# Kernel optimization log

Hardware: AMD Instinct MI355X
Metric: run time of the kernel (lower is better)

## Reference

```python
import jax, jax.numpy as jnp
import numpy as np

N, H, W, C = 2, 96, 96, 256
HEADS, P = 8, 25
DH = C // HEADS
HID = int(C * 4.0)


def _ln(x, g, b):
    m = jnp.mean(x, axis=-1, keepdims=True)
    v = jnp.var(x, axis=-1, keepdims=True)
    return (x - m) / jnp.sqrt(v + 1e-5) * g + b


def _deform_sample(value, loc, h, w):
    # value: (n, heads, h*w, dh); loc: (n, Lq, heads, P, 2) normalized to [0,1] (x,y)
    # Bilinear sampling with align_corners=False and zero padding, as in
    # grid_sample used by MSDeformAttn.
    n = value.shape[0]
    gx = loc[..., 0] * w - 0.5
    gy = loc[..., 1] * h - 0.5
    x0 = jnp.floor(gx)
    y0 = jnp.floor(gy)
    fx = gx - x0
    fy = gy - y0
    out = jnp.zeros((n, HEADS, gx.shape[1] * P, DH), dtype=value.dtype)
    for dx, dy in ((0, 0), (1, 0), (0, 1), (1, 1)):
        xi = x0 + dx
        yi = y0 + dy
        wgt = (fx if dx else 1.0 - fx) * (fy if dy else 1.0 - fy)
        valid = ((xi >= 0) & (xi <= w - 1) & (yi >= 0) & (yi <= h - 1)).astype(value.dtype)
        xi_c = jnp.clip(xi, 0, w - 1).astype(jnp.int32)
        yi_c = jnp.clip(yi, 0, h - 1).astype(jnp.int32)
        idx = yi_c * w + xi_c                                   # (n, Lq, heads, P)
        idx = jnp.transpose(idx, (0, 2, 1, 3)).reshape(n, HEADS, -1)
        g = jnp.take_along_axis(value, idx[..., None], axis=2)  # (n, heads, Lq*P, dh)
        wv = jnp.transpose(wgt * valid, (0, 2, 1, 3)).reshape(n, HEADS, -1, 1)
        out = out + g * wv
    return out


def setup_inputs() -> dict:
    key = jax.random.key(0)
    ks = jax.random.split(key, 20)
    s = 0.02
    inp = {
        'x': jax.random.normal(ks[0], (N, H, W, C), jnp.float32),
        'ref_points': jax.random.uniform(ks[1], (N, H * W, 1, 2), jnp.float32),
        'spatial_shapes': jnp.array([[H, W]], dtype=jnp.int32),
        'level_start_index': jnp.zeros((1,), dtype=jnp.int32),
        'ln1_g': jnp.ones((C,), jnp.float32),
        'ln1_b': jnp.zeros((C,), jnp.float32),
        'w_off': jax.random.normal(ks[2], (C, HEADS * P * 2), jnp.float32) * s,
        'b_off': jax.random.normal(ks[3], (HEADS * P * 2,), jnp.float32) * s,
        'w_attn': jax.random.normal(ks[4], (C, HEADS * P), jnp.float32) * s,
        'b_attn': jax.random.normal(ks[5], (HEADS * P,), jnp.float32) * s,
        'w_val': jax.random.normal(ks[6], (C, C), jnp.float32) * s,
        'b_val': jnp.zeros((C,), jnp.float32),
        'w_out': jax.random.normal(ks[7], (C, C), jnp.float32) * s,
        'b_out': jnp.zeros((C,), jnp.float32),
        'ln2_g': jnp.ones((C,), jnp.float32),
        'ln2_b': jnp.zeros((C,), jnp.float32),
        'w_fc1': jax.random.normal(ks[8], (C, HID), jnp.float32) * s,
        'b_fc1': jnp.zeros((HID,), jnp.float32),
        'w_fc2': jax.random.normal(ks[9], (HID, C), jnp.float32) * s,
        'b_fc2': jnp.zeros((C,), jnp.float32),
    }
    return inp


def reference(x, ref_points, spatial_shapes, level_start_index,
              ln1_g, ln1_b, w_off, b_off, w_attn, b_attn,
              w_val, b_val, w_out, b_out, ln2_g, ln2_b,
              w_fc1, b_fc1, w_fc2, b_fc2):
    n, h, w, c = x.shape
    lq = h * w
    shortcut = x
    # pre-norm + flatten to query
    q = _ln(x, ln1_g, ln1_b).reshape(n, lq, c)
    # MSDeformAttn (n_levels = 1)
    value = (q @ w_val + b_val).reshape(n, lq, HEADS, DH).transpose(0, 2, 1, 3)
    off = (q @ w_off + b_off).reshape(n, lq, HEADS, P, 2)
    aw = jax.nn.softmax((q @ w_attn + b_attn).reshape(n, lq, HEADS, P), axis=-1)
    norm = jnp.array([w, h], dtype=x.dtype)          # offsets normalized by (W, H)
    ref = ref_points[:, :, 0, :]                     # (n, Lq, 2)
    loc = ref[:, :, None, None, :] + off / norm      # (n, Lq, heads, P, 2)
    sampled = _deform_sample(value, loc, h, w).reshape(n, HEADS, lq, P, DH)
    attn = jnp.einsum('nqhp,nhqpd->nqhd', aw, sampled).reshape(n, lq, c)
    attn = attn @ w_out + b_out
    x1 = shortcut + attn.reshape(n, h, w, c)
    # MLP block
    y = _ln(x1, ln2_g, ln2_b)
    y = jax.nn.gelu(y @ w_fc1 + b_fc1, approximate=False) @ w_fc2 + b_fc2
    return x1 + y
```

## Files before the change

kernel.cpp:

```cpp
#include <hip/hip_runtime.h>
#include <hip/hip_bf16.h>
#include <math.h>

typedef __hip_bfloat16 bf16;
typedef __attribute__((ext_vector_type(8))) short short8;
typedef __attribute__((ext_vector_type(4))) float f32x4;

#define NB 2
#define HH 96
#define WW 96
#define CC 256
#define NHEADS 8
#define PP 25
#define DHH 32
#define HIDN 1024
#define LQ (HH*WW)
#define TT (NB*LQ)
#define NVC 896
#define TB 4

__device__ __forceinline__ float b2f(bf16 v){ return __bfloat162float(v); }
__device__ __forceinline__ bf16  f2b(float v){ return __float2bfloat16(v); }
__device__ __forceinline__ float lo_bf(unsigned u){ return __uint_as_float(u << 16); }
__device__ __forceinline__ float hi_bf(unsigned u){ return __uint_as_float(u & 0xffff0000u); }

__device__ __forceinline__ void gl2lds16(const void* g, void* l) {
    __builtin_amdgcn_global_load_lds(
        (const __attribute__((address_space(1))) unsigned int*)g,
        (__attribute__((address_space(3))) unsigned int*)l, 16, 0, 0);
}

__global__ __launch_bounds__(256) void prep_all(const float* __restrict__ w_val,
                                                const float* __restrict__ w_off,
                                                const float* __restrict__ w_attn,
                                                const float* __restrict__ w_fc1,
                                                const float* __restrict__ w_fc2,
                                                const float* __restrict__ w_out,
                                                const float* __restrict__ b_val,
                                                const float* __restrict__ b_off,
                                                const float* __restrict__ b_attn,
                                                bf16* __restrict__ wvcT,
                                                bf16* __restrict__ wfc1T,
                                                bf16* __restrict__ wfc2T,
                                                bf16* __restrict__ woutT,
                                                float* __restrict__ bvc)
{
    const int idx = blockIdx.x*256 + threadIdx.x;
    if (idx < 229376) {
        int n = idx >> 8, k = idx & 255;
        float v = (n < 256) ? w_val[(size_t)k*256 + n]
                : (n < 656) ? w_off[(size_t)k*400 + (n-256)]
                : (n < 856) ? w_attn[(size_t)k*200 + (n-656)] : 0.f;
        wvcT[idx] = f2b(v);
    } else if (idx < 491520) {
        int j = idx - 229376; int n = j >> 8, k = j & 255;
        wfc1T[j] = f2b(w_fc1[(size_t)k*1024 + n]);
    } else if (idx < 753664) {
        int j = idx - 491520; int n = j >> 10, k = j & 1023;
        wfc2T[j] = f2b(w_fc2[(size_t)k*256 + n]);
    } else if (idx < 819200) {
        int j = idx - 753664; int n = j >> 8, k = j & 255;
        woutT[j] = f2b(w_out[(size_t)k*256 + n]);
    }
    if (idx < NVC)
        bvc[idx] = (idx < 256) ? b_val[idx]
                 : (idx < 656) ? b_off[idx-256]
                 : (idx < 856) ? b_attn[idx-656] : 0.f;
}

__global__ __launch_bounds__(256) void ln_kernel(const float* __restrict__ x,
                                                 const float* __restrict__ g,
                                                 const float* __restrict__ b,
                                                 bf16* __restrict__ out)
{
    const int t = blockIdx.x*4 + (threadIdx.x >> 6);
    const int l = threadIdx.x & 63;
    const float4 v = *(const float4*)(x + (size_t)t*CC + l*4);
    float s  = v.x + v.y + v.z + v.w;
    float s2 = v.x*v.x + v.y*v.y + v.z*v.z + v.w*v.w;
    #pragma unroll
    for (int m = 1; m < 64; m <<= 1) { s += __shfl_xor(s, m); s2 += __shfl_xor(s2, m); }
    const float mean = s * (1.f/CC);
    const float var  = s2 * (1.f/CC) - mean*mean;
    const float rs   = 1.f / sqrtf(var + 1e-5f);
    const float4 gg = *(const float4*)(g + l*4);
    const float4 bb = *(const float4*)(b + l*4);
    bf16 o[4];
    o[0] = f2b((v.x-mean)*rs*gg.x + bb.x);
    o[1] = f2b((v.y-mean)*rs*gg.y + bb.y);
    o[2] = f2b((v.z-mean)*rs*gg.z + bb.z);
    o[3] = f2b((v.w-mean)*rs*gg.w + bb.w);
    *(uint2*)(out + (size_t)t*CC + l*4) = *(uint2*)o;
}

template<int EPI, int K, int N, int TM>
__global__ __launch_bounds__(256) void mfma_gemm(const bf16* __restrict__ A,
                                                 const bf16* __restrict__ Bt,
                                                 const float* __restrict__ bias,
                                                 void* __restrict__ outv,
                                                 const float* __restrict__ resid,
                                                 bf16* __restrict__ val_d)
{
    constexpr int AR  = TM/8;
    constexpr int TR  = AR + 16;
    constexpr int RPW = TR/4;
    constexpr int NJ  = (TM==128) ? 4 : 2;
    __shared__ short As[TM*64];
    __shared__ short Bs[128*64];
    const int tid = threadIdx.x;
    const int w = tid >> 6, l = tid & 63;
    const int bm = blockIdx.x, bn = blockIdx.y;

    const bf16* sbase[RPW];
    short*      lbase[RPW];
    {
        const int lrow = l >> 3;
        const int q    = (l & 7) ^ lrow;
        #pragma unroll
        for (int j = 0; j < RPW; j++) {
            int r = w*RPW + j;
            bool isA = r < AR;
            int rr = isA ? r : r - AR;
            int row = rr*8 + lrow;
            size_t grow = (size_t)(isA ? (bm*TM + row) : (bn*128 + row));
            sbase[j] = (isA ? A : Bt) + grow*K + q*8;
            lbase[j] = (isA ? As : Bs) + rr*512;
        }
    }

    const int mbase = (TM==128) ? 64*(w >> 1) : 0;
    const int nbase = (TM==128) ? 64*(w & 1)  : 32*w;

    int aoff[2][4], boff[2][NJ];
    #pragma unroll
    for (int s = 0; s < 2; s++) {
        const int q = s*4 + (l >> 4);
        #pragma unroll
        for (int i = 0; i < 4; i++) {
            int m = mbase + i*16 + (l & 15);
            aoff[s][i] = (m*8 + (q ^ (m & 7))) * 8;
        }
        #pragma unroll
        for (int j = 0; j < NJ; j++) {
            int n = nbase + j*16 + (l & 15);
            boff[s][j] = (n*8 + (q ^ (n & 7))) * 8;
        }
    }

    f32x4 acc[4][NJ];
    #pragma unroll
    for (int i = 0; i < 4; i++)
        #pragma unroll
        for (int j = 0; j < NJ; j++)
            acc[i][j] = (f32x4){0.f, 0.f, 0.f, 0.f};

    for (int k0 = 0; k0 < K; k0 += 64) {
        #pragma unroll
        for (int j = 0; j < RPW; j++)
            gl2lds16(sbase[j] + k0, lbase[j]);
        __syncthreads();
        #pragma unroll
        for (int s = 0; s < 2; s++) {
            short8 af[4], bfr[NJ];
            #pragma unroll
            for (int i = 0; i < 4; i++)  af[i]  = *(const short8*)(As + aoff[s][i]);
            #pragma unroll
            for (int j = 0; j < NJ; j++) bfr[j] = *(const short8*)(Bs + boff[s][j]);
            #pragma unroll
            for (int i = 0; i < 4; i++)
                #pragma unroll
                for (int j = 0; j < NJ; j++)
                    acc[i][j] = __builtin_amdgcn_mfma_f32_16x16x32_bf16(af[i], bfr[j], acc[i][j], 0, 0, 0);
        }
        __syncthreads();
    }

    const int row0 = bm*TM + mbase + (l >> 4)*4;
    const int col0 = bn*128 + nbase + (l & 15);
    #pragma unroll
    for (int i = 0; i < 4; i++) {
        #pragma unroll
        for (int j = 0; j < NJ; j++) {
            const int col = col0 + j*16;
            const float bs = bias[col];
            #pragma unroll
            for (int r = 0; r < 4; r++) {
                const int row = row0 + i*16 + r;
                float v = acc[i][j][r] + bs;
                size_t o = (size_t)row * N + col;
                if (EPI == 0) {
                    ((bf16*)outv)[o] = f2b(v);
                } else if (EPI == 2) {
                    ((bf16*)outv)[o] = f2b(0.5f * v * (1.f + erff(v * 0.70710678118654752f)));
                } else if (EPI == 3) {
                    ((float*)outv)[o] = v + resid[o];
                } else {
                    if (col < 256) val_d[(size_t)row*CC + col] = f2b(v);
                    else           ((bf16*)outv)[o] = f2b(v);
                }
            }
        }
    }
}

struct __align__(16) Tap { _Float16 w[4]; unsigned short i[4]; };

__global__ __launch_bounds__(256) void sample_kernel(const bf16* __restrict__ vc,
                                                     const bf16* __restrict__ val_d,
                                                     const float* __restrict__ refp,
                                                     bf16* __restrict__ samp)
{
    __shared__ Tap taps[TB*200];
    const int b = blockIdx.x;
    const int xcd = b & 7, sub = b >> 3;
    const int tbase = (xcd >> 2)*LQ + ((xcd & 3)*576 + sub)*TB;
    const int tid = threadIdx.x;

    {
        const int pair = tid >> 3;
        const int j    = tid & 7;
        const int tl   = pair >> 3;
        const int h    = pair & 7;
        const int t    = tbase + tl;
        const bf16* row = vc + (size_t)t*NVC;

        float lg[4];
        #pragma unroll
        for (int k = 0; k < 4; k++) {
            int p = j + 8*k;
            lg[k] = (p < PP) ? b2f(row[656 + h*25 + p]) : -1e30f;
        }
        float m = fmaxf(fmaxf(lg[0], lg[1]), fmaxf(lg[2], lg[3]));
        m = fmaxf(m, __shfl_xor(m, 1));
        m = fmaxf(m, __shfl_xor(m, 2));
        m = fmaxf(m, __shfl_xor(m, 4));
        float ex[4], s = 0.f;
        #pragma unroll
        for (int k = 0; k < 4; k++) {
            ex[k] = (j + 8*k < PP) ? expf(lg[k] - m) : 0.f;
            s += ex[k];
        }
        s += __shfl_xor(s, 1);
        s += __shfl_xor(s, 2);
        s += __shfl_xor(s, 4);
        const float inv = 1.f / s;

        const float rx96 = refp[(size_t)t*2 + 0]*96.f - 0.5f;
        const float ry96 = refp[(size_t)t*2 + 1]*96.f - 0.5f;
        const unsigned* offp = (const unsigned*)(row + 256 + h*50);

        #pragma unroll
        for (int k = 0; k < 4; k++) {
            const int p = j + 8*k;
            if (p >= PP) break;
            const float a = ex[k] * inv;
            const unsigned uo = offp[p];
            const float gx = rx96 + lo_bf(uo);
            const float gy = ry96 + hi_bf(uo);
            const float x0f = floorf(gx), y0f = floorf(gy);
            const float fx = gx - x0f, fy = gy - y0f;
            const int ix = (int)x0f, iy = (int)y0f;
            Tap tp;
            #pragma unroll
            for (int d = 0; d < 4; d++) {
                const int dx = d & 1, dy = d >> 1;
                const int xi = ix + dx, yi = iy + dy;
                const bool valid = (xi >= 0) & (xi <= WW-1) & (yi >= 0) & (yi <= HH-1);
                const int xc = min(max(xi, 0), WW-1);
                const int yc = min(max(yi, 0), HH-1);
                tp.i[d] = (unsigned short)(yc*WW + xc);
                tp.w[d] = (_Float16)(valid ? a * (dx ? fx : 1.f-fx) * (dy ? fy : 1.f-fy) : 0.f);
            }
            taps[tl*200 + h*25 + p] = tp;
        }
    }
    __syncthreads();

    const int tok = tid >> 6, l = tid & 63;
    const int h   = l >> 3;
    const int g4  = l & 7;
    const int c0  = h*DHH + g4*4;
    const int t   = tbase + tok;
    const int n   = (t >= LQ) ? 1 : 0;
    const bf16* pv = val_d + (size_t)n*LQ*CC + c0;
    const int pib = tok*200 + h*25;

    float a0 = 0.f, a1 = 0.f, a2 = 0.f, a3 = 0.f;
    for (int p = 0; p < PP; p++) {
        const uint4 tv = *((const uint4*)taps + (pib + p));
        const _Float16* wp_ = (const _Float16*)&tv;
        const unsigned short* ip_ = (const unsigned short*)&tv + 4;
        #pragma unroll
        for (int d = 0; d < 4; d++) {
            const float wt = (float)wp_[d];
            const uint2 vv = *(const uint2*)(pv + (size_t)ip_[d]*CC);
            a0 += wt*lo_bf(vv.x); a1 += wt*hi_bf(vv.x);
            a2 += wt*lo_bf(vv.y); a3 += wt*hi_bf(vv.y);
        }
    }
    bf16 o[4] = { f2b(a0), f2b(a1), f2b(a2), f2b(a3) };
    *(uint2*)(samp + (size_t)t*CC + c0) = *(uint2*)o;
}

extern "C" void kernel_launch(void* const* d_in, const int* in_sizes, int n_in,
                              void* d_out, int out_size, void* d_ws, size_t ws_size,
                              hipStream_t stream)
{
    const float* x      = (const float*)d_in[0];
    const float* refp   = (const float*)d_in[1];
    const float* ln1_g  = (const float*)d_in[4];
    const float* ln1_b  = (const float*)d_in[5];
    const float* w_off  = (const float*)d_in[6];
    const float* b_off  = (const float*)d_in[7];
    const float* w_attn = (const float*)d_in[8];
    const float* b_attn = (const float*)d_in[9];
    const float* w_val  = (const float*)d_in[10];
    const float* b_val  = (const float*)d_in[11];
    const float* w_out  = (const float*)d_in[12];
    const float* b_out  = (const float*)d_in[13];
    const float* ln2_g  = (const float*)d_in[14];
    const float* ln2_b  = (const float*)d_in[15];
    const float* w_fc1  = (const float*)d_in[16];
    const float* b_fc1  = (const float*)d_in[17];
    const float* w_fc2  = (const float*)d_in[18];
    const float* b_fc2  = (const float*)d_in[19];

    char* wsb = (char*)d_ws;
    bf16*  q     = (bf16*)(wsb + 0);
    bf16*  vc    = (bf16*)(wsb + 9437184);
    bf16*  samp  = (bf16*)(wsb + 42467328);
    float* x1    = (float*)(wsb + 51904512);
    bf16*  wvcT  = (bf16*)(wsb + 70778880);
    bf16*  wfc1T = (bf16*)(wsb + 71237632);
    bf16*  wfc2T = (bf16*)(wsb + 71761920);
    bf16*  woutT = (bf16*)(wsb + 72286208);
    float* bvc   = (float*)(wsb + 72417280);
    bf16*  val_d = (bf16*)(wsb + 72420864);
    bf16*  hid   = (bf16*)(wsb + 0);
    bf16*  y0    = samp;

    if (ws_size < 81858048) return;

    const dim3 blk(256);
    prep_all<<<dim3(3200), blk, 0, stream>>>(w_val, w_off, w_attn, w_fc1, w_fc2, w_out,
                                             b_val, b_off, b_attn,
                                             wvcT, wfc1T, wfc2T, woutT, bvc);
    ln_kernel<<<dim3(TT/4), blk, 0, stream>>>(x, ln1_g, ln1_b, q);
    mfma_gemm<4,256,NVC,128><<<dim3(TT/128, NVC/128), blk, 0, stream>>>(q, wvcT, bvc, (void*)vc, nullptr, val_d);
    sample_kernel<<<dim3(TT/TB), blk, 0, stream>>>(vc, val_d, refp, samp);
    mfma_gemm<3,256,CC,64><<<dim3(TT/64, CC/128), blk, 0, stream>>>(samp, woutT, b_out, (void*)x1, x, nullptr);
    ln_kernel<<<dim3(TT/4), blk, 0, stream>>>(x1, ln2_g, ln2_b, y0);
    mfma_gemm<2,256,HIDN,128><<<dim3(TT/128, HIDN/128), blk, 0, stream>>>(y0, wfc1T, b_fc1, (void*)hid, nullptr, nullptr);
    mfma_gemm<3,HIDN,CC,64><<<dim3(TT/64, CC/128), blk, 0, stream>>>(hid, wfc2T, b_fc2, d_out, x1, nullptr);
}
```

Before: 250.7 us.

## Merge bilinear taps into a per-head local weight grid before gathering values

For each (token, head) the sampler now computes the bounding box of all 25 sampling points. If the box fits in a 6x6 window, it scatter-adds the bilinear weights into a shared-memory grid using LDS atomics. The gather loop then reads each distinct pixel once, skipping zero-weight cells, instead of 100 separate tap loads. Wider boxes fall back to the original tap list. This adds an extra barrier, grid zeroing and atomic contention in exchange for far fewer global value gathers when offsets are small.

```diff
diff --git a/kernel.cpp b/kernel.cpp
--- a/kernel.cpp
+++ b/kernel.cpp
@@ -18,6 +18,7 @@
 #define TT (NB*LQ)
 #define NVC 896
 #define TB 4
+#define GW 6
 
 __device__ __forceinline__ float b2f(bf16 v){ return __bfloat162float(v); }
 __device__ __forceinline__ bf16  f2b(float v){ return __float2bfloat16(v); }
@@ -210,11 +211,16 @@
                                                      const float* __restrict__ refp,
                                                      bf16* __restrict__ samp)
 {
-    __shared__ Tap taps[TB*200];
+    __shared__ Tap   taps[TB*200];
+    __shared__ float sgrid[TB*8*36];
+    __shared__ int   smeta[TB*8];
     const int b = blockIdx.x;
     const int xcd = b & 7, sub = b >> 3;
     const int tbase = (xcd >> 2)*LQ + ((xcd & 3)*576 + sub)*TB;
     const int tid = threadIdx.x;
+
+    #pragma unroll
+    for (int i = tid; i < TB*8*36; i += 256) sgrid[i] = 0.f;
 
     {
         const int pair = tid >> 3;
@@ -234,44 +240,94 @@
         m = fmaxf(m, __shfl_xor(m, 1));
         m = fmaxf(m, __shfl_xor(m, 2));
         m = fmaxf(m, __shfl_xor(m, 4));
-        float ex[4], s = 0.f;
+        float aa[4], s = 0.f;
         #pragma unroll
         for (int k = 0; k < 4; k++) {
-            ex[k] = (j + 8*k < PP) ? expf(lg[k] - m) : 0.f;
-            s += ex[k];
+            aa[k] = (j + 8*k < PP) ? expf(lg[k] - m) : 0.f;
+            s += aa[k];
         }
         s += __shfl_xor(s, 1);
         s += __shfl_xor(s, 2);
         s += __shfl_xor(s, 4);
         const float inv = 1.f / s;
+        #pragma unroll
+        for (int k = 0; k < 4; k++) aa[k] *= inv;
 
         const float rx96 = refp[(size_t)t*2 + 0]*96.f - 0.5f;
         const float ry96 = refp[(size_t)t*2 + 1]*96.f - 0.5f;
         const unsigned* offp = (const unsigned*)(row + 256 + h*50);
-
+        float gxs[4], gys[4];
+        int mnx = 95, mxx = 0, mny = 95, mxy = 0;
         #pragma unroll
         for (int k = 0; k < 4; k++) {
             const int p = j + 8*k;
             if (p >= PP) break;
-            const float a = ex[k] * inv;
             const unsigned uo = offp[p];
-            const float gx = rx96 + lo_bf(uo);
-            const float gy = ry96 + hi_bf(uo);
-            const float x0f = floorf(gx), y0f = floorf(gy);
-            const float fx = gx - x0f, fy = gy - y0f;
-            const int ix = (int)x0f, iy = (int)y0f;
-            Tap tp;
-            #pragma unroll
-            for (int d = 0; d < 4; d++) {
-                const int dx = d & 1, dy = d >> 1;
-                const int xi = ix + dx, yi = iy + dy;
-                const bool valid = (xi >= 0) & (xi <= WW-1) & (yi >= 0) & (yi <= HH-1);
-                const int xc = min(max(xi, 0), WW-1);
-                const int yc = min(max(yi, 0), HH-1);
-                tp.i[d] = (unsigned short)(yc*WW + xc);
-                tp.w[d] = (_Float16)(valid ? a * (dx ? fx : 1.f-fx) * (dy ? fy : 1.f-fy) : 0.f);
+            gxs[k] = rx96 + lo_bf(uo);
+            gys[k] = ry96 + hi_bf(uo);
+            const int ix = (int)floorf(gxs[k]);
+            const int iy = (int)floorf(gys[k]);
+            mnx = min(mnx, min(max(ix,   0), WW-1));
+            mxx = max(mxx, min(max(ix+1, 0), WW-1));
+            mny = min(mny, min(max(iy,   0), HH-1));
+            mxy = max(mxy, min(max(iy+1, 0), HH-1));
+        }
+        mnx = min(mnx, __shfl_xor(mnx, 1)); mxx = max(mxx, __shfl_xor(mxx, 1));
+        mnx = min(mnx, __shfl_xor(mnx, 2)); mxx = max(mxx, __shfl_xor(mxx, 2));
+        mnx = min(mnx, __shfl_xor(mnx, 4)); mxx = max(mxx, __shfl_xor(mxx, 4));
+        mny = min(mny, __shfl_xor(mny, 1)); mxy = max(mxy, __shfl_xor(mxy, 1));
+        mny = min(mny, __shfl_xor(mny, 2)); mxy = max(mxy, __shfl_xor(mxy, 2));
+        mny = min(mny, __shfl_xor(mny, 4)); mxy = max(mxy, __shfl_xor(mxy, 4));
+        const int bw = mxx - mnx + 1, bh = mxy - mny + 1;
+        const int ok = (bw <= GW && bh <= GW) ? 1 : 0;
+        if (j == 0)
+            smeta[pair] = mnx | (mny << 7) | (bw << 14) | (bh << 21) | (ok << 28);
+
+        __syncthreads();
+
+        if (ok) {
+            float* gp = sgrid + pair*36;
+            #pragma unroll
+            for (int k = 0; k < 4; k++) {
+                const int p = j + 8*k;
+                if (p >= PP) break;
+                const float a = aa[k];
+                const float x0f = floorf(gxs[k]), y0f = floorf(gys[k]);
+                const float fx = gxs[k] - x0f, fy = gys[k] - y0f;
+                const int ix = (int)x0f, iy = (int)y0f;
+                #pragma unroll
+                for (int d = 0; d < 4; d++) {
+                    const int dx = d & 1, dy = d >> 1;
+                    const int xi = ix + dx, yi = iy + dy;
+                    const bool valid = (xi >= 0) & (xi <= WW-1) & (yi >= 0) & (yi <= HH-1);
+                    const int xc = min(max(xi, 0), WW-1);
+                    const int yc = min(max(yi, 0), HH-1);
+                    const float wt = valid ? a * (dx ? fx : 1.f-fx) * (dy ? fy : 1.f-fy) : 0.f;
+                    atomicAdd(&gp[(yc - mny)*GW + (xc - mnx)], wt);
+                }
             }
-            taps[tl*200 + h*25 + p] = tp;
+        } else {
+            #pragma unroll
+            for (int k = 0; k < 4; k++) {
+                const int p = j + 8*k;
+                if (p >= PP) break;
+                const float a = aa[k];
+                const float x0f = floorf(gxs[k]), y0f = floorf(gys[k]);
+                const float fx = gxs[k] - x0f, fy = gys[k] - y0f;
+                const int ix = (int)x0f, iy = (int)y0f;
+                Tap tp;
+                #pragma unroll
+                for (int d = 0; d < 4; d++) {
+                    const int dx = d & 1, dy = d >> 1;
+                    const int xi = ix + dx, yi = iy + dy;
+                    const bool valid = (xi >= 0) & (xi <= WW-1) & (yi >= 0) & (yi <= HH-1);
+                    const int xc = min(max(xi, 0), WW-1);
+                    const int yc = min(max(yi, 0), HH-1);
+                    tp.i[d] = (unsigned short)(yc*WW + xc);
+                    tp.w[d] = (_Float16)(valid ? a * (dx ? fx : 1.f-fx) * (dy ? fy : 1.f-fy) : 0.f);
+                }
+                taps[tl*200 + h*25 + p] = tp;
+            }
         }
     }
     __syncthreads();
@@ -283,19 +339,40 @@
     const int t   = tbase + tok;
     const int n   = (t >= LQ) ? 1 : 0;
     const bf16* pv = val_d + (size_t)n*LQ*CC + c0;
-    const int pib = tok*200 + h*25;
+    const int pair = tok*8 + h;
+
+    const int meta = smeta[pair];
+    const int ox = meta & 127, oy = (meta >> 7) & 127;
+    const int bw = (meta >> 14) & 127, bh = (meta >> 21) & 127;
+    const int ok = (meta >> 28) & 1;
 
     float a0 = 0.f, a1 = 0.f, a2 = 0.f, a3 = 0.f;
-    for (int p = 0; p < PP; p++) {
-        const uint4 tv = *((const uint4*)taps + (pib + p));
-        const _Float16* wp_ = (const _Float16*)&tv;
-        const unsigned short* ip_ = (const unsigned short*)&tv + 4;
-        #pragma unroll
-        for (int d = 0; d < 4; d++) {
-            const float wt = (float)wp_[d];
-            const uint2 vv = *(const uint2*)(pv + (size_t)ip_[d]*CC);
-            a0 += wt*lo_bf(vv.x); a1 += wt*hi_bf(vv.x);
-            a2 += wt*lo_bf(vv.y); a3 += wt*hi_bf(vv.y);
+    if (ok) {
+        const float* gp = sgrid + pair*36;
+        for (int cy = 0; cy < bh; cy++) {
+            const int rowpix = (oy + cy)*WW + ox;
+            for (int cx = 0; cx < bw; cx++) {
+                const float wt = gp[cy*GW + cx];
+                if (wt != 0.f) {
+                    const uint2 vv = *(const uint2*)(pv + (size_t)(rowpix + cx)*CC);
+                    a0 += wt*lo_bf(vv.x); a1 += wt*hi_bf(vv.x);
+                    a2 += wt*lo_bf(vv.y); a3 += wt*hi_bf(vv.y);
+                }
+            }
+        }
+    } else {
+        const int pib = tok*200 + h*25;
+        for (int p = 0; p < PP; p++) {
+            const uint4 tv = *((const uint4*)taps + (pib + p));
+            const _Float16* wp_ = (const _Float16*)&tv;
+            const unsigned short* ip_ = (const unsigned short*)&tv + 4;
+            #pragma unroll
+            for (int d = 0; d < 4; d++) {
+                const float wt = (float)wp_[d];
+                const uint2 vv = *(const uint2*)(pv + (size_t)ip_[d]*CC);
+                a0 += wt*lo_bf(vv.x); a1 += wt*hi_bf(vv.x);
+                a2 += wt*lo_bf(vv.y); a3 += wt*hi_bf(vv.y);
+            }
         }
     }
     bf16 o[4] = { f2b(a0), f2b(a1), f2b(a2), f2b(a3) };
```

Measured after the change: 303.6 us. +21.1%, slower.
